# Kernel tuning notes

Measured on AMD Instinct MI355X. Metric: run time of the kernel, lower is better.

Reference implementation:

```python
import jax, jax.numpy as jnp
import numpy as np

D = 1024
H = 16
HD = D // H


def setup_inputs() -> dict:
    key = jax.random.key(0)
    ks = jax.random.split(key, 9)
    s = 1.0 / np.sqrt(D)
    x = jax.random.normal(ks[0], (2, 2048, D), dtype=jnp.float32)
    Wq = jax.random.uniform(ks[1], (D, D), jnp.float32, -s, s)
    bq = jax.random.uniform(ks[2], (D,), jnp.float32, -s, s)
    Wk = jax.random.uniform(ks[3], (D, D), jnp.float32, -s, s)
    bk = jax.random.uniform(ks[4], (D,), jnp.float32, -s, s)
    Wv = jax.random.uniform(ks[5], (D, D), jnp.float32, -s, s)
    bv = jax.random.uniform(ks[6], (D,), jnp.float32, -s, s)
    Wo = jax.random.uniform(ks[7], (D, D), jnp.float32, -s, s)
    bo = jax.random.uniform(ks[8], (D,), jnp.float32, -s, s)
    return {"x": x, "Wq": Wq, "bq": bq, "Wk": Wk, "bk": bk,
            "Wv": Wv, "bv": bv, "Wo": Wo, "bo": bo}


def reference(x, Wq, bq, Wk, bk, Wv, bv, Wo, bo):
    B, S, _ = x.shape
    # project and split heads -> [B, H, S, HD]
    def split(t):
        return t.reshape(B, S, H, HD).transpose(0, 2, 1, 3)
    q = split(x @ Wq + bq)
    k = split(x @ Wk + bk)
    v = split(x @ Wv + bv)
    scores = jnp.einsum('bhqd,bhkd->bhqk', q, k) / np.sqrt(HD).astype(np.float32)
    attn = jax.nn.softmax(scores, axis=-1)
    ctx = jnp.einsum('bhqk,bhkd->bhqd', attn, v)  # [B,H,S,HD]
    ctx = ctx.transpose(0, 2, 1, 3).reshape(B, S, D)
    return ctx @ Wo + bo
```

## Files before the change

kernel.cpp:

```cpp
#include <hip/hip_runtime.h>
#include <hip/hip_bf16.h>
#include <math.h>

#define BB 2
#define SS 2048
#define DD 1024
#define HH 16
#define HD 64
#define MM (BB * SS)
#define NT (SS / 64)

typedef __bf16 bf16;
typedef __attribute__((ext_vector_type(8))) __bf16 bf16x8;
typedef __attribute__((ext_vector_type(4))) __bf16 bf16x4;
typedef __attribute__((ext_vector_type(4))) float f32x4;
typedef __attribute__((ext_vector_type(4))) unsigned u32x4;

#define QSCL 0.18033688011112042f

__device__ __forceinline__ void glds16(const bf16* g, bf16* l) {
    __builtin_amdgcn_global_load_lds(
        (const __attribute__((address_space(1))) void*)g,
        (__attribute__((address_space(3))) void*)l, 16, 0, 0);
}

__device__ __forceinline__ unsigned cvtpk_bf16(float a, float b) {
    unsigned r;
    asm("v_cvt_pk_bf16_f32 %0, %1, %2" : "=v"(r) : "v"(a), "v"(b));
    return r;
}

__device__ __forceinline__ float exp2p(float s) {
    float n = rintf(s);
    float f = s - n;
    float p = fmaf(f, 0.00961812910f, 0.0555041087f);
    p = fmaf(f, p, 0.240226507f);
    p = fmaf(f, p, 0.693147180f);
    p = fmaf(f, p, 1.0f);
    return ldexpf(p, (int)n);
}

__global__ __launch_bounds__(256) void cvt_prep(
    const float* __restrict__ x, bf16* __restrict__ xb,
    const float* __restrict__ W0, const float* __restrict__ W1,
    const float* __restrict__ W2, const float* __restrict__ W3,
    bf16* __restrict__ Wt) {
    __shared__ float T[64][65];
    const int bid = blockIdx.x;
    if (bid < 4096) {
        int i = (bid * 256 + threadIdx.x) * 4;
        float4 v = *(const float4*)(x + i);
        bf16x4 o;
        o[0] = (bf16)v.x; o[1] = (bf16)v.y; o[2] = (bf16)v.z; o[3] = (bf16)v.w;
        *(bf16x4*)(xb + i) = o;
        return;
    }
    const int b = bid - 4096;
    const int z = b >> 8;
    const float* W = (z == 0) ? W0 : (z == 1) ? W1 : (z == 2) ? W2 : W3;
    bf16* dst = Wt + (size_t)z * DD * DD;
    int k0 = ((b >> 4) & 15) * 64, n0 = (b & 15) * 64;
    int tr = threadIdx.x >> 4, tc = (threadIdx.x & 15) * 4;
#pragma unroll
    for (int u = 0; u < 4; u++) {
        int r = tr + u * 16;
        float4 v = *(const float4*)&W[(size_t)(k0 + r) * DD + n0 + tc];
        T[tc + 0][r] = v.x; T[tc + 1][r] = v.y;
        T[tc + 2][r] = v.z; T[tc + 3][r] = v.w;
    }
    __syncthreads();
#pragma unroll
    for (int u = 0; u < 4; u++) {
        int r = tr + u * 16;
        bf16x4 o;
        o[0] = (bf16)T[r][tc + 0]; o[1] = (bf16)T[r][tc + 1];
        o[2] = (bf16)T[r][tc + 2]; o[3] = (bf16)T[r][tc + 3];
        *(bf16x4*)&dst[(size_t)(n0 + r) * DD + k0 + tc] = o;
    }
}

__global__ __launch_bounds__(512, 2) void mfma_gemm_qkv(
    const bf16* __restrict__ A, const bf16* __restrict__ Wt0,
    const float* __restrict__ b0, const float* __restrict__ b1,
    const float* __restrict__ b2,
    bf16* __restrict__ o0, bf16* __restrict__ o1, bf16* __restrict__ o2) {
    __shared__ __align__(16) bf16 As[2][256 * 64];
    __shared__ __align__(16) bf16 Bs[2][256 * 64];

    const int lin = blockIdx.x;
    const int nl = (lin & 7) * 24 + (lin >> 3);
    const int mt = nl & 15;
    const int nt = nl >> 4;
    const int m0 = mt * 256;
    const int n0g = nt * 256;
    const int z = n0g >> 10;
    const int n0 = n0g & 1023;
    const bf16* Wt = Wt0 + (size_t)z * DD * DD + (size_t)n0 * DD;
    const float* bias = (z == 0) ? b0 : (z == 1) ? b1 : b2;
    const float scl = (z == 0) ? QSCL : 1.0f;

    const int tid = threadIdx.x;
    const int lane = tid & 63;
    const int w = tid >> 6;
    const int wm = w >> 2;
    const int wn = w & 3;
    const int l15 = lane & 15, quad = lane >> 4;

    const bf16* gA[4]; const bf16* gB[4]; int loff[4];
#pragma unroll
    for (int u = 0; u < 4; u++) {
        int j = tid + u * 512;
        int r = j >> 3, cp = j & 7;
        int c = cp ^ (r & 7);
        gA[u] = A  + (size_t)(m0 + r) * DD + c * 8;
        gB[u] = Wt + (size_t)r * DD + c * 8;
        loff[u] = j * 8;
    }

    f32x4 acc[8][4];
#pragma unroll
    for (int i = 0; i < 8; i++)
#pragma unroll
        for (int j = 0; j < 4; j++) acc[i][j] = (f32x4){0.f, 0.f, 0.f, 0.f};

#pragma unroll
    for (int u = 0; u < 4; u++) {
        glds16(gA[u], &As[0][loff[u]]);  gA[u] += 64;
        glds16(gB[u], &Bs[0][loff[u]]);  gB[u] += 64;
    }
    __syncthreads();

    for (int t = 0; t < DD / 64; ++t) {
        const int buf = t & 1;
        if (t + 1 < DD / 64) {
#pragma unroll
            for (int u = 0; u < 4; u++) {
                glds16(gA[u], &As[buf ^ 1][loff[u]]);  gA[u] += 64;
                glds16(gB[u], &Bs[buf ^ 1][loff[u]]);  gB[u] += 64;
            }
        }
        __builtin_amdgcn_s_setprio(1);
#pragma unroll
        for (int kh = 0; kh < 2; kh++) {
            bf16x8 bfr[4];
#pragma unroll
            for (int j = 0; j < 4; j++) {
                int rb = wn * 64 + j * 16 + l15;
                bfr[j] = *(const bf16x8*)
                    &Bs[buf][rb * 64 + (((kh * 4 + quad) ^ (rb & 7)) << 3)];
            }
#pragma unroll
            for (int i = 0; i < 8; i++) {
                int ra = wm * 128 + i * 16 + l15;
                bf16x8 afr = *(const bf16x8*)
                    &As[buf][ra * 64 + (((kh * 4 + quad) ^ (ra & 7)) << 3)];
#pragma unroll
                for (int j = 0; j < 4; j++)
                    acc[i][j] = __builtin_amdgcn_mfma_f32_16x16x32_bf16(
                        afr, bfr[j], acc[i][j], 0, 0, 0);
            }
        }
        __builtin_amdgcn_s_setprio(0);
        __syncthreads();
    }

    float bcol[4];
#pragma unroll
    for (int j = 0; j < 4; j++) bcol[j] = bias[n0 + wn * 64 + j * 16 + l15];

    if (z == 2) {
#pragma unroll
        for (int i = 0; i < 8; i++) {
            const int g = i >> 2, ig = i & 3;
            const int mb64 = m0 + wm * 128 + g * 64;
            const int bb = (mb64 >= SS) ? 1 : 0;
            const int sw = mb64 & (SS - 1);
            const int scol = sw + (ig >> 1) * 32 + quad * 8 + (ig & 1) * 4;
#pragma unroll
            for (int j = 0; j < 4; j++) {
                int dg = n0 + wn * 64 + j * 16 + l15;
                int h = dg >> 6, d = dg & 63;
                bf16* dst = o2 + ((size_t)(bb * HH + h) * HD + d) * SS + scol;
                bf16x4 ov;
#pragma unroll
                for (int r = 0; r < 4; r++)
                    ov[r] = (bf16)(acc[i][j][r] + bcol[j]);
                *(bf16x4*)dst = ov;
            }
        }
    } else {
        bf16* dstb = (z == 0) ? o0 : o1;
#pragma unroll
        for (int i = 0; i < 8; i++)
#pragma unroll
            for (int j = 0; j < 4; j++)
#pragma unroll
                for (int r = 0; r < 4; r++) {
                    int row = m0 + wm * 128 + i * 16 + quad * 4 + r;
                    int col = n0 + wn * 64 + j * 16 + l15;
                    dstb[(size_t)row * DD + col] =
                        (bf16)((acc[i][j][r] + bcol[j]) * scl);
                }
    }
}

__global__ __launch_bounds__(256) void mfma_gemm_out(
    const bf16* __restrict__ A, const bf16* __restrict__ Wt,
    const float* __restrict__ bias, float* __restrict__ out) {
    const int lin = blockIdx.x;
    const int nl = (lin & 7) * 64 + (lin >> 3);
    const int m0 = (nl >> 3) * 64;
    const int n0 = (nl & 7) * 128;

    __shared__ __align__(16) bf16 As[64 * 64];
    __shared__ __align__(16) bf16 Bs[128 * 64];

    const int tid = threadIdx.x;
    const int lane = tid & 63;
    const int w = tid >> 6;
    const int l15 = lane & 15, quad = lane >> 4;
    const int mw = (w & 1) * 32;
    const int nw = (w >> 1) * 64;

    f32x4 acc[2][4];
#pragma unroll
    for (int i = 0; i < 2; i++)
#pragma unroll
        for (int j = 0; j < 4; j++) acc[i][j] = (f32x4){0.f, 0.f, 0.f, 0.f};

    for (int kt = 0; kt < DD; kt += 64) {
        __syncthreads();
#pragma unroll
        for (int u = 0; u < 2; u++) {
            int j = tid + u * 256;
            int row = j >> 3, c = (j & 7) ^ (row & 7);
            glds16(A + (size_t)(m0 + row) * DD + kt + c * 8, &As[j * 8]);
        }
#pragma unroll
        for (int u = 0; u < 4; u++) {
            int j = tid + u * 256;
            int row = j >> 3, c = (j & 7) ^ (row & 7);
            glds16(Wt + (size_t)(n0 + row) * DD + kt + c * 8, &Bs[j * 8]);
        }
        __syncthreads();

#pragma unroll
        for (int kh = 0; kh < 2; kh++) {
            bf16x8 af[2], bf[4];
#pragma unroll
            for (int i = 0; i < 2; i++) {
                int ra = mw + i * 16 + l15;
                int ja = ra * 8 + ((kh * 4 + quad) ^ (ra & 7));
                af[i] = *(const bf16x8*)&As[ja * 8];
            }
#pragma unroll
            for (int j = 0; j < 4; j++) {
                int rb = nw + j * 16 + l15;
                int jb = rb * 8 + ((kh * 4 + quad) ^ (rb & 7));
                bf[j] = *(const bf16x8*)&Bs[jb * 8];
            }
#pragma unroll
            for (int i = 0; i < 2; i++)
#pragma unroll
                for (int j = 0; j < 4; j++)
                    acc[i][j] = __builtin_amdgcn_mfma_f32_16x16x32_bf16(
                        af[i], bf[j], acc[i][j], 0, 0, 0);
        }
    }

    float bcol[4];
#pragma unroll
    for (int j = 0; j < 4; j++) bcol[j] = bias[n0 + nw + j * 16 + l15];

#pragma unroll
    for (int i = 0; i < 2; i++)
#pragma unroll
        for (int j = 0; j < 4; j++)
#pragma unroll
            for (int r = 0; r < 4; r++) {
                int row = m0 + mw + i * 16 + quad * 4 + r;
                int col = n0 + nw + j * 16 + l15;
                out[(size_t)row * DD + col] = acc[i][j][r] + bcol[j];
            }
}

__global__ __launch_bounds__(256) void mfma_attn(
    const bf16* __restrict__ Qb, const bf16* __restrict__ Kb,
    const bf16* __restrict__ Vtg, bf16* __restrict__ ctxb) {
    __shared__ __align__(16) bf16 Ks[2][64 * 64];
    __shared__ __align__(16) bf16 Vs[2][64 * 64];

    const int lin = blockIdx.x;
    const int nl = (lin & 7) * 128 + (lin >> 3);
    const int bh = nl >> 5;
    const int q0 = (nl & 31) * 64;

    const int tid = threadIdx.x;
    const int lane = tid & 63;
    const int w = tid >> 6;
    const int l15 = lane & 15, quad = lane >> 4;
    const int b = bh >> 4, h = bh & 15;
    const size_t mb = (size_t)b * SS;
    const int hc = h * HD;
    const bf16* Vt_bh = Vtg + (size_t)bh * HD * SS;

    bf16x8 qf[2];
#pragma unroll
    for (int kh = 0; kh < 2; kh++)
        qf[kh] = *(const bf16x8*)&Qb[(mb + q0 + w * 16 + l15) * DD +
                                     hc + kh * 32 + quad * 8];

    bf16x8 onev;
#pragma unroll
    for (int i = 0; i < 8; i++) onev[i] = (bf16)1.0f;
    const f32x4 zf = (f32x4){0.f, 0.f, 0.f, 0.f};

    int koff[4][2], voff[4][2];
#pragma unroll
    for (int kb = 0; kb < 4; kb++) {
        int rk = kb * 16 + l15;
#pragma unroll
        for (int kh = 0; kh < 2; kh++)
            koff[kb][kh] = (rk * 8 + ((kh * 4 + quad) ^ (rk & 7))) * 8;
    }
#pragma unroll
    for (int nb = 0; nb < 4; nb++) {
        int rv = nb * 16 + l15;
#pragma unroll
        for (int kh = 0; kh < 2; kh++)
            voff[nb][kh] = (rv * 8 + ((kh * 4 + quad) ^ (rv & 7))) * 8;
    }

    const bf16* gK[2]; const bf16* gV[2]; int lo_[2];
#pragma unroll
    for (int u = 0; u < 2; u++) {
        int j = tid + u * 256;
        int row = j >> 3, cp = j & 7;
        int c = cp ^ (row & 7);
        gK[u] = Kb + (mb + row) * DD + hc + c * 8;
        gV[u] = Vt_bh + (size_t)row * SS + c * 8;
        lo_[u] = j * 8;
    }

    f32x4 o[4], lsum;
    lsum = (f32x4){0.f, 0.f, 0.f, 0.f};
#pragma unroll
    for (int nb = 0; nb < 4; nb++) o[nb] = (f32x4){0.f, 0.f, 0.f, 0.f};

#pragma unroll
    for (int u = 0; u < 2; u++) {
        glds16(gK[u], &Ks[0][lo_[u]]);  gK[u] += 64 * DD;
        glds16(gV[u], &Vs[0][lo_[u]]);  gV[u] += 64;
    }
    __syncthreads();

    f32x4 scA[4];
#pragma unroll
    for (int kb = 0; kb < 4; kb++) {
        bf16x8 kf0 = *(const bf16x8*)&Ks[0][koff[kb][0]];
        bf16x8 kf1 = *(const bf16x8*)&Ks[0][koff[kb][1]];
        f32x4 t = __builtin_amdgcn_mfma_f32_16x16x32_bf16(
            kf0, qf[0], zf, 0, 0, 0);
        scA[kb] = __builtin_amdgcn_mfma_f32_16x16x32_bf16(
            kf1, qf[1], t, 0, 0, 0);
    }

    int buf = 0;
    for (int it = 0; it < NT; ++it) {
        const bool more = (it + 1 < NT);
        if (more) {
#pragma unroll
            for (int u = 0; u < 2; u++) {
                glds16(gK[u], &Ks[buf ^ 1][lo_[u]]);  gK[u] += 64 * DD;
                glds16(gV[u], &Vs[buf ^ 1][lo_[u]]);  gV[u] += 64;
            }
        }

        u32x4 pw[2];
#pragma unroll
        for (int kb = 0; kb < 4; kb++) {
            float p0 = exp2p(scA[kb][0]);
            float p1 = exp2p(scA[kb][1]);
            float p2 = exp2p(scA[kb][2]);
            float p3 = exp2p(scA[kb][3]);
            pw[kb >> 1][(kb & 1) * 2 + 0] = cvtpk_bf16(p0, p1);
            pw[kb >> 1][(kb & 1) * 2 + 1] = cvtpk_bf16(p2, p3);
        }
        bf16x8 pfr[2];
        pfr[0] = __builtin_bit_cast(bf16x8, pw[0]);
        pfr[1] = __builtin_bit_cast(bf16x8, pw[1]);

        __syncthreads();

        __builtin_amdgcn_s_setprio(1);
        f32x4 scB[4];
        if (more) {
#pragma unroll
            for (int kb = 0; kb < 4; kb++) {
                bf16x8 kf0 = *(const bf16x8*)&Ks[buf ^ 1][koff[kb][0]];
                bf16x8 kf1 = *(const bf16x8*)&Ks[buf ^ 1][koff[kb][1]];
                f32x4 t = __builtin_amdgcn_mfma_f32_16x16x32_bf16(
                    kf0, qf[0], zf, 0, 0, 0);
                scB[kb] = __builtin_amdgcn_mfma_f32_16x16x32_bf16(
                    kf1, qf[1], t, 0, 0, 0);
            }
        }
#pragma unroll
        for (int kh = 0; kh < 2; kh++) {
            lsum = __builtin_amdgcn_mfma_f32_16x16x32_bf16(
                pfr[kh], onev, lsum, 0, 0, 0);
#pragma unroll
            for (int nb = 0; nb < 4; nb++) {
                bf16x8 vf = *(const bf16x8*)&Vs[buf][voff[nb][kh]];
                o[nb] = __builtin_amdgcn_mfma_f32_16x16x32_bf16(
                    pfr[kh], vf, o[nb], 0, 0, 0);
            }
        }
        __builtin_amdgcn_s_setprio(0);

        __syncthreads();

        if (more) {
#pragma unroll
            for (int kb = 0; kb < 4; kb++) scA[kb] = scB[kb];
        }
        buf ^= 1;
    }

    float li[4];
#pragma unroll
    for (int r = 0; r < 4; r++) li[r] = 1.0f / lsum[r];
#pragma unroll
    for (int nb = 0; nb < 4; nb++)
#pragma unroll
        for (int r = 0; r < 4; r++) {
            int qrow = q0 + w * 16 + quad * 4 + r;
            ctxb[(mb + qrow) * DD + hc + nb * 16 + l15] =
                (bf16)(o[nb][r] * li[r]);
        }
}

extern "C" void kernel_launch(void* const* d_in, const int* in_sizes, int n_in,
                              void* d_out, int out_size, void* d_ws, size_t ws_size,
                              hipStream_t stream) {
    const float* x  = (const float*)d_in[0];
    const float* Wq = (const float*)d_in[1];
    const float* bq = (const float*)d_in[2];
    const float* Wk = (const float*)d_in[3];
    const float* bk = (const float*)d_in[4];
    const float* Wv = (const float*)d_in[5];
    const float* bv = (const float*)d_in[6];
    const float* Wo = (const float*)d_in[7];
    const float* bo = (const float*)d_in[8];
    float* out = (float*)d_out;

    char* base = (char*)d_ws;
    bf16* xb   = (bf16*)(base);
    bf16* Wt   = (bf16*)(base + (8ull  << 20));
    bf16* Qb   = (bf16*)(base + (16ull << 20));
    bf16* Kb   = (bf16*)(base + (24ull << 20));
    bf16* Vt   = (bf16*)(base + (32ull << 20));
    bf16* ctxb = (bf16*)(base + (40ull << 20));

    cvt_prep<<<dim3(4096 + 1024), dim3(256), 0, stream>>>(
        x, xb, Wq, Wk, Wv, Wo, Wt);

    mfma_gemm_qkv<<<dim3(192), dim3(512), 0, stream>>>(
        xb, Wt, bq, bk, bv, Qb, Kb, Vt);

    mfma_attn<<<dim3(1024), dim3(256), 0, stream>>>(Qb, Kb, Vt, ctxb);

    mfma_gemm_out<<<dim3(512), dim3(256), 0, stream>>>(
        ctxb, Wt + 3ull * DD * DD, bo, out);
}
```

Measured before the change: 203.7 us.

## Double-buffer LDS tiles in output projection GEMM to overlap loads with MFMA

The output-projection GEMM now keeps two LDS buffers for the A and B tiles. It issues the global-to-LDS loads for the next K tile before running the MFMAs on the current one, which cuts one barrier per iteration and hides load latency. Global pointers are precomputed once and advanced each step, and s_setprio raises wave priority around the MFMA block. LDS use doubles, which may reduce occupancy.

```diff
diff --git a/kernel.cpp b/kernel.cpp
--- a/kernel.cpp
+++ b/kernel.cpp
@@ -207,13 +207,13 @@
 __global__ __launch_bounds__(256) void mfma_gemm_out(
     const bf16* __restrict__ A, const bf16* __restrict__ Wt,
     const float* __restrict__ bias, float* __restrict__ out) {
+    __shared__ __align__(16) bf16 As[2][64 * 64];
+    __shared__ __align__(16) bf16 Bs[2][128 * 64];
+
     const int lin = blockIdx.x;
     const int nl = (lin & 7) * 64 + (lin >> 3);
     const int m0 = (nl >> 3) * 64;
     const int n0 = (nl & 7) * 128;
-
-    __shared__ __align__(16) bf16 As[64 * 64];
-    __shared__ __align__(16) bf16 Bs[128 * 64];
 
     const int tid = threadIdx.x;
     const int lane = tid & 63;
@@ -222,28 +222,49 @@
     const int mw = (w & 1) * 32;
     const int nw = (w >> 1) * 64;
 
+    const bf16* gA[2]; int loA[2];
+#pragma unroll
+    for (int u = 0; u < 2; u++) {
+        int j = tid + u * 256;
+        int r = j >> 3, c = (j & 7) ^ (r & 7);
+        gA[u] = A + (size_t)(m0 + r) * DD + c * 8;
+        loA[u] = j * 8;
+    }
+    const bf16* gB[4]; int loB[4];
+#pragma unroll
+    for (int u = 0; u < 4; u++) {
+        int j = tid + u * 256;
+        int r = j >> 3, c = (j & 7) ^ (r & 7);
+        gB[u] = Wt + (size_t)(n0 + r) * DD + c * 8;
+        loB[u] = j * 8;
+    }
+
     f32x4 acc[2][4];
 #pragma unroll
     for (int i = 0; i < 2; i++)
 #pragma unroll
         for (int j = 0; j < 4; j++) acc[i][j] = (f32x4){0.f, 0.f, 0.f, 0.f};
 
-    for (int kt = 0; kt < DD; kt += 64) {
-        __syncthreads();
-#pragma unroll
-        for (int u = 0; u < 2; u++) {
-            int j = tid + u * 256;
-            int row = j >> 3, c = (j & 7) ^ (row & 7);
-            glds16(A + (size_t)(m0 + row) * DD + kt + c * 8, &As[j * 8]);
-        }
-#pragma unroll
-        for (int u = 0; u < 4; u++) {
-            int j = tid + u * 256;
-            int row = j >> 3, c = (j & 7) ^ (row & 7);
-            glds16(Wt + (size_t)(n0 + row) * DD + kt + c * 8, &Bs[j * 8]);
-        }
-        __syncthreads();
-
+#pragma unroll
+    for (int u = 0; u < 2; u++) { glds16(gA[u], &As[0][loA[u]]); gA[u] += 64; }
+#pragma unroll
+    for (int u = 0; u < 4; u++) { glds16(gB[u], &Bs[0][loB[u]]); gB[u] += 64; }
+    __syncthreads();
+
+    for (int t = 0; t < DD / 64; ++t) {
+        const int buf = t & 1;
+        if (t + 1 < DD / 64) {
+#pragma unroll
+            for (int u = 0; u < 2; u++) {
+                glds16(gA[u], &As[buf ^ 1][loA[u]]);  gA[u] += 64;
+            }
+#pragma unroll
+            for (int u = 0; u < 4; u++) {
+                glds16(gB[u], &Bs[buf ^ 1][loB[u]]);  gB[u] += 64;
+            }
+        }
+
+        __builtin_amdgcn_s_setprio(1);
 #pragma unroll
         for (int kh = 0; kh < 2; kh++) {
             bf16x8 af[2], bf[4];
@@ -251,13 +272,13 @@
             for (int i = 0; i < 2; i++) {
                 int ra = mw + i * 16 + l15;
                 int ja = ra * 8 + ((kh * 4 + quad) ^ (ra & 7));
-                af[i] = *(const bf16x8*)&As[ja * 8];
+                af[i] = *(const bf16x8*)&As[buf][ja * 8];
             }
 #pragma unroll
             for (int j = 0; j < 4; j++) {
                 int rb = nw + j * 16 + l15;
                 int jb = rb * 8 + ((kh * 4 + quad) ^ (rb & 7));
-                bf[j] = *(const bf16x8*)&Bs[jb * 8];
+                bf[j] = *(const bf16x8*)&Bs[buf][jb * 8];
             }
 #pragma unroll
             for (int i = 0; i < 2; i++)
@@ -266,6 +287,8 @@
                     acc[i][j] = __builtin_amdgcn_mfma_f32_16x16x32_bf16(
                         af[i], bf[j], acc[i][j], 0, 0, 0);
         }
+        __builtin_amdgcn_s_setprio(0);
+        __syncthreads();
     }
 
     float bcol[4];
```

Result: slower. 212.0 us (+4.1%).

## Retile fused QKV GEMM to 256x192 tiles so 256 blocks fill all CUs

Applied to the files above, without the earlier changes.

The fused QKV projection GEMM now uses 256x192 output tiles instead of 256x256, which raises the grid from 192 to 256 workgroups to match the 256 CUs of the MI355X. Because a 192-wide tile can straddle the Q/K/V boundaries, the epilogue now picks bias, scale and output layout per 16-column fragment instead of per block. The aim is to remove the partial-wave tail where only 192 CUs were busy. In exchange each block does less MFMA work per A-tile load and has a more branchy epilogue.

```diff
diff --git a/kernel.cpp b/kernel.cpp
--- a/kernel.cpp
+++ b/kernel.cpp
@@ -85,19 +85,14 @@
     const float* __restrict__ b2,
     bf16* __restrict__ o0, bf16* __restrict__ o1, bf16* __restrict__ o2) {
     __shared__ __align__(16) bf16 As[2][256 * 64];
-    __shared__ __align__(16) bf16 Bs[2][256 * 64];
+    __shared__ __align__(16) bf16 Bs[2][192 * 64];
 
     const int lin = blockIdx.x;
-    const int nl = (lin & 7) * 24 + (lin >> 3);
+    const int nl = (lin & 7) * 32 + (lin >> 3);
     const int mt = nl & 15;
     const int nt = nl >> 4;
     const int m0 = mt * 256;
-    const int n0g = nt * 256;
-    const int z = n0g >> 10;
-    const int n0 = n0g & 1023;
-    const bf16* Wt = Wt0 + (size_t)z * DD * DD + (size_t)n0 * DD;
-    const float* bias = (z == 0) ? b0 : (z == 1) ? b1 : b2;
-    const float scl = (z == 0) ? QSCL : 1.0f;
+    const int n0g = nt * 192;
 
     const int tid = threadIdx.x;
     const int lane = tid & 63;
@@ -106,28 +101,35 @@
     const int wn = w & 3;
     const int l15 = lane & 15, quad = lane >> 4;
 
-    const bf16* gA[4]; const bf16* gB[4]; int loff[4];
+    const bf16* gA[4]; int loA[4];
 #pragma unroll
     for (int u = 0; u < 4; u++) {
         int j = tid + u * 512;
         int r = j >> 3, cp = j & 7;
         int c = cp ^ (r & 7);
-        gA[u] = A  + (size_t)(m0 + r) * DD + c * 8;
-        gB[u] = Wt + (size_t)r * DD + c * 8;
-        loff[u] = j * 8;
-    }
-
-    f32x4 acc[8][4];
+        gA[u] = A + (size_t)(m0 + r) * DD + c * 8;
+        loA[u] = j * 8;
+    }
+    const bf16* gB[3]; int loB[3];
+#pragma unroll
+    for (int u = 0; u < 3; u++) {
+        int j = tid + u * 512;
+        int r = j >> 3, cp = j & 7;
+        int c = cp ^ (r & 7);
+        gB[u] = Wt0 + (size_t)(n0g + r) * DD + c * 8;
+        loB[u] = j * 8;
+    }
+
+    f32x4 acc[8][3];
 #pragma unroll
     for (int i = 0; i < 8; i++)
 #pragma unroll
-        for (int j = 0; j < 4; j++) acc[i][j] = (f32x4){0.f, 0.f, 0.f, 0.f};
-
-#pragma unroll
-    for (int u = 0; u < 4; u++) {
-        glds16(gA[u], &As[0][loff[u]]);  gA[u] += 64;
-        glds16(gB[u], &Bs[0][loff[u]]);  gB[u] += 64;
-    }
+        for (int j = 0; j < 3; j++) acc[i][j] = (f32x4){0.f, 0.f, 0.f, 0.f};
+
+#pragma unroll
+    for (int u = 0; u < 4; u++) { glds16(gA[u], &As[0][loA[u]]); gA[u] += 64; }
+#pragma unroll
+    for (int u = 0; u < 3; u++) { glds16(gB[u], &Bs[0][loB[u]]); gB[u] += 64; }
     __syncthreads();
 
     for (int t = 0; t < DD / 64; ++t) {
@@ -135,17 +137,20 @@
         if (t + 1 < DD / 64) {
 #pragma unroll
             for (int u = 0; u < 4; u++) {
-                glds16(gA[u], &As[buf ^ 1][loff[u]]);  gA[u] += 64;
-                glds16(gB[u], &Bs[buf ^ 1][loff[u]]);  gB[u] += 64;
+                glds16(gA[u], &As[buf ^ 1][loA[u]]);  gA[u] += 64;
+            }
+#pragma unroll
+            for (int u = 0; u < 3; u++) {
+                glds16(gB[u], &Bs[buf ^ 1][loB[u]]);  gB[u] += 64;
             }
         }
         __builtin_amdgcn_s_setprio(1);
 #pragma unroll
         for (int kh = 0; kh < 2; kh++) {
-            bf16x8 bfr[4];
-#pragma unroll
-            for (int j = 0; j < 4; j++) {
-                int rb = wn * 64 + j * 16 + l15;
+            bf16x8 bfr[3];
+#pragma unroll
+            for (int j = 0; j < 3; j++) {
+                int rb = wn * 48 + j * 16 + l15;
                 bfr[j] = *(const bf16x8*)
                     &Bs[buf][rb * 64 + (((kh * 4 + quad) ^ (rb & 7)) << 3)];
             }
@@ -155,7 +160,7 @@
                 bf16x8 afr = *(const bf16x8*)
                     &As[buf][ra * 64 + (((kh * 4 + quad) ^ (ra & 7)) << 3)];
 #pragma unroll
-                for (int j = 0; j < 4; j++)
+                for (int j = 0; j < 3; j++)
                     acc[i][j] = __builtin_amdgcn_mfma_f32_16x16x32_bf16(
                         afr, bfr[j], acc[i][j], 0, 0, 0);
             }
@@ -164,43 +169,41 @@
         __syncthreads();
     }
 
-    float bcol[4];
-#pragma unroll
-    for (int j = 0; j < 4; j++) bcol[j] = bias[n0 + wn * 64 + j * 16 + l15];
-
-    if (z == 2) {
-#pragma unroll
-        for (int i = 0; i < 8; i++) {
-            const int g = i >> 2, ig = i & 3;
-            const int mb64 = m0 + wm * 128 + g * 64;
-            const int bb = (mb64 >= SS) ? 1 : 0;
-            const int sw = mb64 & (SS - 1);
-            const int scol = sw + (ig >> 1) * 32 + quad * 8 + (ig & 1) * 4;
-#pragma unroll
-            for (int j = 0; j < 4; j++) {
-                int dg = n0 + wn * 64 + j * 16 + l15;
-                int h = dg >> 6, d = dg & 63;
+#pragma unroll
+    for (int j = 0; j < 3; j++) {
+        const int colg = n0g + wn * 48 + j * 16 + l15;
+        const int zj = colg >> 10;
+        const int cz = colg & 1023;
+        const float* bj = (zj == 0) ? b0 : (zj == 1) ? b1 : b2;
+        const float bc = bj[cz];
+        if (zj == 2) {
+            const int h = cz >> 6, d = cz & 63;
+#pragma unroll
+            for (int i = 0; i < 8; i++) {
+                const int g = i >> 2, ig = i & 3;
+                const int mb64 = m0 + wm * 128 + g * 64;
+                const int bb = (mb64 >= SS) ? 1 : 0;
+                const int sw = mb64 & (SS - 1);
+                const int scol = sw + (ig >> 1) * 32 + quad * 8 + (ig & 1) * 4;
                 bf16* dst = o2 + ((size_t)(bb * HH + h) * HD + d) * SS + scol;
                 bf16x4 ov;
 #pragma unroll
                 for (int r = 0; r < 4; r++)
-                    ov[r] = (bf16)(acc[i][j][r] + bcol[j]);
+                    ov[r] = (bf16)(acc[i][j][r] + bc);
                 *(bf16x4*)dst = ov;
             }
-        }
-    } else {
-        bf16* dstb = (z == 0) ? o0 : o1;
-#pragma unroll
-        for (int i = 0; i < 8; i++)
-#pragma unroll
-            for (int j = 0; j < 4; j++)
+        } else {
+            bf16* dstb = (zj == 0) ? o0 : o1;
+            const float scl = (zj == 0) ? QSCL : 1.0f;
+#pragma unroll
+            for (int i = 0; i < 8; i++)
 #pragma unroll
                 for (int r = 0; r < 4; r++) {
                     int row = m0 + wm * 128 + i * 16 + quad * 4 + r;
-                    int col = n0 + wn * 64 + j * 16 + l15;
-                    dstb[(size_t)row * DD + col] =
-                        (bf16)((acc[i][j][r] + bcol[j]) * scl);
+                    dstb[(size_t)row * DD + cz] =
+                        (bf16)((acc[i][j][r] + bc) * scl);
                 }
+        }
     }
 }
 
@@ -465,7 +468,7 @@
     cvt_prep<<<dim3(4096 + 1024), dim3(256), 0, stream>>>(
         x, xb, Wq, Wk, Wv, Wo, Wt);
 
-    mfma_gemm_qkv<<<dim3(192), dim3(512), 0, stream>>>(
+    mfma_gemm_qkv<<<dim3(256), dim3(512), 0, stream>>>(
         xb, Wt, bq, bk, bv, Qb, Kb, Vt);
 
     mfma_attn<<<dim3(1024), dim3(256), 0, stream>>>(Qb, Kb, Vt, ctxb);
```

Result: no change. 206.1 us (+1.1%).
